# Kernel optimization log

Hardware: AMD Instinct MI355X
Metric: run time of the kernel (lower is better)

## Reference

```python
import jax, jax.numpy as jnp
import numpy as np

# Config (matches init_kwargs)
B, C, H, W = 32, 128, 12, 1200   # z: (B, in_dim, H, W)
DIN = C * H                       # 1536
FIX = 768                         # get_multiple(DIN // 2, 6)
OV = 4                            # overlap
G = 6                             # num_vqs
D = OV * FIX // G                 # 512 per-group embedding size (all equal)
K = 1024                          # codebook_size
COMMIT = 0.25


def setup_inputs() -> dict:
    key = jax.random.key(0)
    k1, k2, k3, k4 = jax.random.split(key, 4)
    z = jax.random.normal(k1, (B, C, H, W), dtype=jnp.float32)
    w_down = jax.random.normal(k2, (FIX, DIN), dtype=jnp.float32) * 0.02
    w_up = jax.random.normal(k3, (DIN, FIX), dtype=jnp.float32) * 0.02
    embedding = jax.random.normal(k4, (G, D, K), dtype=jnp.float32)  # per-group (embedding_size, num_embedding)
    return {"z": z, "w_down": w_down, "w_up": w_up, "embedding": embedding}


def _quantize_group(zg, emb):
    # zg: (B, T, D), emb: (D, K)
    zf = zg.reshape(-1, D)
    # squared euclidean distance: |z|^2 - 2 z@E + |E|^2 -> (N, K)
    dist = (zf * zf).sum(1, keepdims=True) - 2.0 * (zf @ emb) + (emb * emb).sum(0, keepdims=True)
    idx = jnp.argmin(dist, axis=1)            # (N,)
    q = jnp.take(emb.T, idx, axis=0).reshape(zg.shape)
    # straight-through estimator (training mode)
    zq = zg + jax.lax.stop_gradient(q - zg)
    loss = COMMIT * jnp.mean((jax.lax.stop_gradient(zq) - zg) ** 2)
    return zq, loss


def reference(z, w_down, w_up, embedding):
    # pre_process: (B,C,H,W) -> permute(0,2,3,1) -> permute(0,2,3,1) -> (B, W, C*H)
    x = jnp.transpose(z, (0, 3, 1, 2)).reshape(B, W, DIN)  # (B, W, C, H) flattened
    x = x @ w_down.T                                       # proj_down -> (B, W, FIX)
    T = W // OV
    x = x.reshape(B, T, OV * FIX)                          # (B, T, 3072)
    # split into G contiguous groups of size D along last axis -> (G, B, T, D)
    xg = jnp.transpose(x.reshape(B, T, G, D), (2, 0, 1, 3))
    zq_g, losses = jax.vmap(_quantize_group)(xg, embedding)
    vq_loss = losses.sum() / G
    # concat groups back -> (B, T, G*D)
    zq = jnp.transpose(zq_g, (1, 2, 0, 3)).reshape(B, T, G * D)
    # post_process: un-overlap, proj_up, back to (B, C, H, W)
    zq = zq.reshape(B, W, FIX)
    zq = zq @ w_up.T                                       # (B, W, DIN)
    zq = zq.reshape(B, W, C, H)
    zq = jnp.transpose(zq, (0, 3, 1, 2))                   # (B, H, W, C)
    zq = jnp.transpose(zq, (0, 3, 1, 2))                   # dim==4 -> (B, C, H, W)
    return zq, vq_loss
```

## Files before the change

kernel.cpp:

```cpp
#include <hip/hip_runtime.h>

#define BB 32
#define CC 128
#define HH 12
#define WW 1200
#define DIN 1536
#define FIXD 768
#define OVL 4
#define GG 6
#define DD 512
#define KK 1024
#define TT 300
#define NV 9600
#define MROWS 38400

#define Y_OFF     0
#define ET_OFF    29491200
#define NORM_OFF  32636928
#define BEST_OFF  32643072
#define LOSS_OFF  32758272
#define ZN_OFF    32758336
#define UMIN_OFF  32815936
#define CNT_OFF   32873536
#define MAXN_OFF  32931136
#define LIST_OFF  32931200
#define YBF_OFF   36617600
#define EBF_OFF   51363200

#define BSWZ(c) ((c) + 4 * ((c) >> 5))

typedef __attribute__((ext_vector_type(8))) short bf16x8;
typedef __attribute__((ext_vector_type(4))) float f32x4;

static __device__ inline unsigned short f2bf(float x) {
    unsigned u = __float_as_uint(x);
    unsigned r = (u + 0x7fffu + ((u >> 16) & 1u)) >> 16;
    return (unsigned short)r;
}
static __device__ inline unsigned enc32(float s) {
    unsigned u = __float_as_uint(s);
    return (u & 0x80000000u) ? ~u : (u | 0x80000000u);
}

__global__ __launch_bounds__(256) void k_gemm_down(const float* __restrict__ z,
                                                   const float* __restrict__ w_down,
                                                   float* __restrict__ Y) {
    __shared__ float As[16][132];
    __shared__ float Bs[16][140];
    const int n0 = blockIdx.y * 128, f0 = blockIdx.x * 128;
    const int tid = threadIdx.x;
    const int arow = tid & 127;
    const int ak0 = tid >> 7;
    const int nA = n0 + arow;
    const int bA = nA / WW, wA = nA - bA * WW;
    const size_t zbase = (size_t)bA * (CC * HH * WW) + wA;
    const int bcol = tid >> 1, bq = tid & 1;
    const int bsc = BSWZ(bcol);
    const int trow = tid >> 4, tcol = tid & 15;
    const int bread = tcol * 8 + 4 * (tcol >> 2);
    float acc[8][8] = {};
    for (int kt = 0; kt < DIN; kt += 16) {
        #pragma unroll
        for (int i = 0; i < 8; i++) {
            const int kk = ak0 + i * 2;
            As[kk][arow] = z[zbase + (size_t)(kt + kk) * WW];
        }
        #pragma unroll
        for (int i = 0; i < 2; i++) {
            const int q = bq + i * 2;
            const float4 v = *(const float4*)&w_down[(size_t)(f0 + bcol) * DIN + kt + q * 4];
            Bs[q * 4 + 0][bsc] = v.x;
            Bs[q * 4 + 1][bsc] = v.y;
            Bs[q * 4 + 2][bsc] = v.z;
            Bs[q * 4 + 3][bsc] = v.w;
        }
        __syncthreads();
        #pragma unroll
        for (int k = 0; k < 16; k++) {
            float av[8], bv[8];
            *(float4*)&av[0] = *(const float4*)&As[k][trow * 8];
            *(float4*)&av[4] = *(const float4*)&As[k][trow * 8 + 4];
            *(float4*)&bv[0] = *(const float4*)&Bs[k][bread];
            *(float4*)&bv[4] = *(const float4*)&Bs[k][bread + 4];
            #pragma unroll
            for (int i = 0; i < 8; i++)
                #pragma unroll
                for (int j = 0; j < 8; j++)
                    acc[i][j] = fmaf(av[i], bv[j], acc[i][j]);
        }
        __syncthreads();
    }
    #pragma unroll
    for (int i = 0; i < 8; i++) {
        float4 o0, o1;
        o0.x = acc[i][0]; o0.y = acc[i][1]; o0.z = acc[i][2]; o0.w = acc[i][3];
        o1.x = acc[i][4]; o1.y = acc[i][5]; o1.z = acc[i][6]; o1.w = acc[i][7];
        float* yr = &Y[(size_t)(n0 + trow * 8 + i) * FIXD + f0 + tcol * 8];
        *(float4*)yr = o0;
        *(float4*)(yr + 4) = o1;
    }
}

__global__ __launch_bounds__(256) void k_transpose(const float* __restrict__ emb,
                                                   float* __restrict__ ET) {
    int i = blockIdx.x * 256 + threadIdx.x;
    if (i >= GG * KK * DD) return;
    int d = i & 511;
    int rem = i >> 9;
    int k = rem & 1023;
    int g = rem >> 10;
    ET[i] = emb[((g * DD + d) << 10) + k];
}

__global__ __launch_bounds__(64) void k_norms(const float* __restrict__ ET,
                                              float* __restrict__ norms,
                                              unsigned* __restrict__ maxnU) {
    const int code = blockIdx.x;
    const int lane = threadIdx.x;
    const float* row = ET + code * DD;
    double s = 0.0;
    #pragma unroll
    for (int r = 0; r < 8; r++) {
        float v = row[lane + r * 64];
        s += (double)v * (double)v;
    }
    #pragma unroll
    for (int off = 32; off; off >>= 1) s += __shfl_down(s, off);
    if (lane == 0) {
        const float nf = (float)s;
        norms[code] = nf;
        atomicMax(&maxnU[code >> 10], __float_as_uint(nf));
    }
}

__global__ __launch_bounds__(256) void k_ysplit(const float* __restrict__ Y,
                                                unsigned short* __restrict__ Ybf,
                                                float* __restrict__ znorm) {
    const int gv = blockIdx.x * 4 + (threadIdx.x >> 6);
    const int lane = threadIdx.x & 63;
    const int g = gv / NV, r = gv - g * NV;
    const int b = r / TT, t = r - b * TT;
    const int d0 = lane * 8;
    const int p = g * DD + d0;
    const int sg = p / FIXD, f = p - sg * FIXD;
    const float* yb = &Y[(size_t)((b * WW + t * OVL + sg) * FIXD + f)];
    const float4 y0 = *(const float4*)yb;
    const float4 y1 = *(const float4*)(yb + 4);
    unsigned short h[8];
    h[0] = f2bf(y0.x); h[1] = f2bf(y0.y); h[2] = f2bf(y0.z); h[3] = f2bf(y0.w);
    h[4] = f2bf(y1.x); h[5] = f2bf(y1.y); h[6] = f2bf(y1.z); h[7] = f2bf(y1.w);
    *(uint4*)&Ybf[(size_t)gv * DD + d0] = *(uint4*)&h[0];
    float s = 0.f;
    s = fmaf(y0.x, y0.x, s); s = fmaf(y0.y, y0.y, s);
    s = fmaf(y0.z, y0.z, s); s = fmaf(y0.w, y0.w, s);
    s = fmaf(y1.x, y1.x, s); s = fmaf(y1.y, y1.y, s);
    s = fmaf(y1.z, y1.z, s); s = fmaf(y1.w, y1.w, s);
    #pragma unroll
    for (int off = 32; off; off >>= 1) s += __shfl_down(s, off);
    if (lane == 0) znorm[gv] = s;
}

__global__ __launch_bounds__(256) void k_esplit(const float* __restrict__ ET,
                                                unsigned short* __restrict__ Ebf) {
    const size_t i8 = ((size_t)blockIdx.x * 256 + threadIdx.x) * 8;
    const float4 a = *(const float4*)&ET[i8];
    const float4 b = *(const float4*)&ET[i8 + 4];
    unsigned short h[8];
    h[0] = f2bf(a.x); h[1] = f2bf(a.y); h[2] = f2bf(a.z); h[3] = f2bf(a.w);
    h[4] = f2bf(b.x); h[5] = f2bf(b.y); h[6] = f2bf(b.z); h[7] = f2bf(b.w);
    *(uint4*)&Ebf[i8] = *(uint4*)&h[0];
}

template<int PHASE>
__global__ __launch_bounds__(256) void k_dist3(const unsigned short* __restrict__ Ybf,
                                               const unsigned short* __restrict__ Ebf,
                                               const float* __restrict__ norms,
                                               const float* __restrict__ znorm,
                                               const unsigned* __restrict__ maxnU,
                                               unsigned* __restrict__ umin,
                                               unsigned* __restrict__ cnt,
                                               unsigned* __restrict__ list_) {
    __shared__ unsigned short Ah[128][40], Bh[128][40];
    __shared__ float a1s[128], margs[128];
    const int ct = blockIdx.x;
    const int vt = blockIdx.y;
    const int g  = blockIdx.z;
    const int v0 = vt * 128, c0 = ct * 128;
    const int tid = threadIdx.x;
    const size_t ybase = ((size_t)g * NV + v0) * DD;
    const size_t ebase = ((size_t)g * KK + c0) * DD;
    const int srow = tid >> 1, sseg = (tid & 1) * 16;
    const int wv = tid >> 6, lane = tid & 63;
    const int wr = wv >> 1, wc = wv & 1;
    const int m0 = wr * 64, n0 = wc * 64;
    const int lr = lane & 15, lq = lane >> 4;

    if (PHASE == 2 && tid < 128) {
        const int gv = g * NV + v0 + tid;
        const unsigned u = umin[gv];
        const unsigned x = (u & 0x80000000u) ? (u & 0x7fffffffu) : ~u;
        a1s[tid] = __uint_as_float(x);
        margs[tid] = 0.032f * sqrtf(znorm[gv] * __uint_as_float(maxnU[g]));
    }

    f32x4 acc[4][4];
    #pragma unroll
    for (int i = 0; i < 4; i++)
        #pragma unroll
        for (int j = 0; j < 4; j++) acc[i][j] = (f32x4){0.f, 0.f, 0.f, 0.f};

    for (int kt = 0; kt < DD; kt += 32) {
        {
            const uint4 a0 = *(const uint4*)&Ybf[ybase + (size_t)srow * DD + kt + sseg];
            const uint4 a1 = *(const uint4*)&Ybf[ybase + (size_t)srow * DD + kt + sseg + 8];
            const uint4 b0 = *(const uint4*)&Ebf[ebase + (size_t)srow * DD + kt + sseg];
            const uint4 b1 = *(const uint4*)&Ebf[ebase + (size_t)srow * DD + kt + sseg + 8];
            *(uint4*)&Ah[srow][sseg]     = a0;
            *(uint4*)&Ah[srow][sseg + 8] = a1;
            *(uint4*)&Bh[srow][sseg]     = b0;
            *(uint4*)&Bh[srow][sseg + 8] = b1;
        }
        __syncthreads();
        bf16x8 ah[4], bh[4];
        #pragma unroll
        for (int i = 0; i < 4; i++) {
            ah[i] = *(bf16x8*)&Ah[m0 + i * 16 + lr][lq * 8];
            bh[i] = *(bf16x8*)&Bh[n0 + i * 16 + lr][lq * 8];
        }
        #pragma unroll
        for (int i = 0; i < 4; i++)
            #pragma unroll
            for (int j = 0; j < 4; j++)
                acc[i][j] = __builtin_amdgcn_mfma_f32_16x16x32_bf16(ah[i], bh[j], acc[i][j], 0, 0, 0);
        __syncthreads();
    }

    float nrmj[4];
    #pragma unroll
    for (int j = 0; j < 4; j++) nrmj[j] = norms[(g << 10) + c0 + n0 + j * 16 + lr];

    #pragma unroll
    for (int i = 0; i < 4; i++) {
        #pragma unroll
        for (int rr = 0; rr < 4; rr++) {
            const int row = m0 + i * 16 + lq * 4 + rr;
            if (PHASE == 1) {
                unsigned kb = 0xFFFFFFFFu;
                #pragma unroll
                for (int j = 0; j < 4; j++) {
                    const unsigned u = enc32(nrmj[j] - 2.0f * acc[i][j][rr]);
                    kb = (u < kb) ? u : kb;
                }
                #pragma unroll
                for (int off = 1; off < 16; off <<= 1) {
                    const unsigned o = __shfl_xor(kb, off);
                    kb = (o < kb) ? o : kb;
                }
                if (lr == 0) atomicMin(&umin[g * NV + v0 + row], kb);
            } else {
                const float thr = a1s[row] + margs[row];
                #pragma unroll
                for (int j = 0; j < 4; j++) {
                    const float sc = nrmj[j] - 2.0f * acc[i][j][rr];
                    if (sc <= thr) {
                        const int gv = g * NV + v0 + row;
                        const unsigned idx = atomicAdd(&cnt[gv], 1u);
                        if (idx < 64u)
                            list_[(size_t)gv * 64 + idx] = (unsigned)(c0 + n0 + j * 16 + lr);
                    }
                }
            }
        }
    }
}

__global__ __launch_bounds__(64) void k_rescore(const float* __restrict__ Y,
                                                const float* __restrict__ ET,
                                                const float* __restrict__ norms,
                                                const unsigned* __restrict__ cnt,
                                                const unsigned* __restrict__ list_,
                                                unsigned long long* __restrict__ best) {
    const int gv = blockIdx.x;
    const unsigned n = cnt[gv];
    if (n == 0u || n > 64u) return;
    const int lane = threadIdx.x;
    const int g = gv / NV, r = gv - g * NV;
    const int b = r / TT, t = r - b * TT;
    unsigned long long key = ~0ull;
    if (lane < (int)n) {
        const unsigned c = list_[(size_t)gv * 64 + lane];
        const float* erow = &ET[((size_t)((g << 10) + c)) * DD];
        float s = 0.f;
        for (int d4 = 0; d4 < 128; ++d4) {
            const int p = g * DD + d4 * 4;
            const int sg = p / FIXD, f = p - sg * FIXD;
            const float4 yv = *(const float4*)&Y[(size_t)((b * WW + t * OVL + sg) * FIXD + f)];
            const float4 ev = *(const float4*)&erow[d4 * 4];
            s = fmaf(yv.x, ev.x, s); s = fmaf(yv.y, ev.y, s);
            s = fmaf(yv.z, ev.z, s); s = fmaf(yv.w, ev.w, s);
        }
        const float sc = norms[(g << 10) + c] - 2.0f * s;
        key = ((unsigned long long)enc32(sc) << 32) | c;
    }
    #pragma unroll
    for (int off = 32; off; off >>= 1) {
        const unsigned long long o = __shfl_down(key, off);
        if (o < key) key = o;
    }
    if (lane == 0) best[gv] = key;
}

__global__ __launch_bounds__(256) void k_fallback(const float* __restrict__ Y,
                                                  const float* __restrict__ ET,
                                                  const float* __restrict__ norms,
                                                  const unsigned* __restrict__ cnt,
                                                  unsigned long long* __restrict__ best) {
    const int gv = blockIdx.x;
    if (cnt[gv] <= 64u) return;
    __shared__ float Yv[512];
    __shared__ unsigned long long red[256];
    const int tid = threadIdx.x;
    const int g = gv / NV, r = gv - g * NV;
    const int b = r / TT, t = r - b * TT;
    if (tid < 128) {
        const int p = g * DD + tid * 4;
        const int sg = p / FIXD, f = p - sg * FIXD;
        *(float4*)&Yv[tid * 4] = *(const float4*)&Y[(size_t)((b * WW + t * OVL + sg) * FIXD + f)];
    }
    __syncthreads();
    unsigned long long kb = ~0ull;
    for (int cc = 0; cc < 4; ++cc) {
        const int c = tid + cc * 256;
        const float* erow = &ET[((size_t)((g << 10) + c)) * DD];
        float s = 0.f;
        for (int d = 0; d < 512; ++d) s = fmaf(Yv[d], erow[d], s);
        const float sc = norms[(g << 10) + c] - 2.0f * s;
        const unsigned long long key = ((unsigned long long)enc32(sc) << 32) | (unsigned)c;
        if (key < kb) kb = key;
    }
    red[tid] = kb;
    __syncthreads();
    for (int off = 128; off; off >>= 1) {
        if (tid < off) { if (red[tid + off] < red[tid]) red[tid] = red[tid + off]; }
        __syncthreads();
    }
    if (tid == 0) best[gv] = red[0];
}

__global__ __launch_bounds__(256) void k_sumloss(const unsigned long long* __restrict__ best,
                                                 const float* __restrict__ znorm,
                                                 float* __restrict__ lossAcc) {
    const int v = blockIdx.x * 256 + threadIdx.x;
    const unsigned long long key = best[v];
    const unsigned u = (unsigned)(key >> 32);
    const unsigned x = (u & 0x80000000u) ? (u & 0x7fffffffu) : ~u;
    float s = __uint_as_float(x) + znorm[v];
    __shared__ float red[256];
    red[threadIdx.x] = s;
    __syncthreads();
    for (int off = 128; off; off >>= 1) {
        if (threadIdx.x < off) red[threadIdx.x] += red[threadIdx.x + off];
        __syncthreads();
    }
    if (threadIdx.x == 0) atomicAdd(lossAcc, red[0]);
}

__constant__ int SEG_G[8]  = {0, 1, 1, 2, 3, 4, 4, 5};
__constant__ int SEG_D0[8] = {0, 0, 256, 0, 0, 0, 256, 0};
__constant__ int SEG_L[8]  = {512, 256, 256, 512, 512, 256, 256, 512};
__constant__ int SEG_F0[8] = {0, 512, 0, 256, 0, 512, 0, 256};

__global__ __launch_bounds__(256) void k_table(const float* __restrict__ ET,
                                               const float* __restrict__ w_up,
                                               float* __restrict__ Tab) {
    __shared__ float As[16][68];
    __shared__ float Bs[16][140];
    const int bm = blockIdx.x;
    const int bn = blockIdx.y;
    const int seg = blockIdx.z;
    const int g = SEG_G[seg], d0 = SEG_D0[seg], len = SEG_L[seg], fb = SEG_F0[seg];
    const int tid = threadIdx.x;
    const int k0 = bm * 64, dout0 = bn * 128;
    const int arow = tid >> 2, aq = tid & 3;
    const int rbase = (tid >> 4) << 2;
    const int cgrp = tid & 15;
    const int bread = cgrp * 8 + 4 * (cgrp >> 2);
    const float* ETg = ET + (size_t)(g << 10) * DD;
    float acc[4][8] = {};
    for (int kt = 0; kt < len; kt += 16) {
        {
            const float4 v = *(const float4*)&ETg[(size_t)(k0 + arow) * DD + d0 + kt + aq * 4];
            As[aq * 4 + 0][arow] = v.x;
            As[aq * 4 + 1][arow] = v.y;
            As[aq * 4 + 2][arow] = v.z;
            As[aq * 4 + 3][arow] = v.w;
        }
        #pragma unroll
        for (int i = 0; i < 2; i++) {
            int fl = tid + i * 256;
            int col = fl >> 2, q = fl & 3;
            const int sc = BSWZ(col);
            const float4 v = *(const float4*)&w_up[(size_t)(dout0 + col) * FIXD + fb + kt + q * 4];
            Bs[q * 4 + 0][sc] = v.x;
            Bs[q * 4 + 1][sc] = v.y;
            Bs[q * 4 + 2][sc] = v.z;
            Bs[q * 4 + 3][sc] = v.w;
        }
        __syncthreads();
        #pragma unroll
        for (int k = 0; k < 16; k++) {
            const float4 a  = *(const float4*)&As[k][rbase];
            const float4 ba = *(const float4*)&Bs[k][bread];
            const float4 bb = *(const float4*)&Bs[k][bread + 4];
            const float av[4] = {a.x, a.y, a.z, a.w};
            const float bv[8] = {ba.x, ba.y, ba.z, ba.w, bb.x, bb.y, bb.z, bb.w};
            #pragma unroll
            for (int i = 0; i < 4; i++)
                #pragma unroll
                for (int j = 0; j < 8; j++)
                    acc[i][j] = fmaf(av[i], bv[j], acc[i][j]);
        }
        __syncthreads();
    }
    #pragma unroll
    for (int i = 0; i < 4; i++) {
        float4 o0, o1;
        o0.x = acc[i][0]; o0.y = acc[i][1]; o0.z = acc[i][2]; o0.w = acc[i][3];
        o1.x = acc[i][4]; o1.y = acc[i][5]; o1.z = acc[i][6]; o1.w = acc[i][7];
        float* tr = &Tab[(size_t)((seg << 10) + k0 + rbase + i) * DIN + dout0 + cgrp * 8];
        *(float4*)tr = o0;
        *(float4*)(tr + 4) = o1;
    }
}

__global__ __launch_bounds__(256) void k_scatter(const float* __restrict__ Tab,
                                                 const unsigned long long* __restrict__ best,
                                                 float* __restrict__ out) {
    __shared__ float Ls[64][65];
    const int dt = blockIdx.x;
    const int wt = blockIdx.y;
    const int b  = blockIdx.z;
    const int dout0 = dt * 64, w0 = wt * 64;
    const int wlim = (WW - w0 < 64) ? (WW - w0) : 64;
    const int tid = threadIdx.x;
    const int wi = tid >> 2, q = tid & 3;

    if (wi < wlim) {
        const int w = w0 + wi;
        const int s = w & 3;
        const int t = w >> 2;
        const int gEt[4] = {0, 1, 3, 4};
        const int gOt[4] = {1, 2, 4, 5};
        int ce = (int)(unsigned)best[gEt[s] * NV + b * TT + t];
        int co = (int)(unsigned)best[gOt[s] * NV + b * TT + t];
        size_t rowE = (size_t)(((2 * s) << 10) + ce) * DIN;
        size_t rowO = (size_t)(((2 * s + 1) << 10) + co) * DIN;
        #pragma unroll
        for (int rep = 0; rep < 4; rep++) {
            const int doff = rep * 16 + q * 4;
            const float4 a = *(const float4*)&Tab[rowE + dout0 + doff];
            const float4 c = *(const float4*)&Tab[rowO + dout0 + doff];
            Ls[wi][doff + 0] = a.x + c.x;
            Ls[wi][doff + 1] = a.y + c.y;
            Ls[wi][doff + 2] = a.z + c.z;
            Ls[wi][doff + 3] = a.w + c.w;
        }
    }
    __syncthreads();
    const size_t obase = (size_t)b * (CC * HH * WW) + (size_t)dout0 * WW + w0;
    #pragma unroll
    for (int i = 0; i < 16; i++) {
        int flat = tid + i * 256;
        int dr = flat >> 6, wj = flat & 63;
        if (wj < wlim) out[obase + (size_t)dr * WW + wj] = Ls[wj][dr];
    }
}

__global__ void k_finish(const float* __restrict__ lossAcc, float* __restrict__ out) {
    if (threadIdx.x == 0)
        out[58982400] = lossAcc[0] * (0.25f / 29491200.0f);
}

extern "C" void kernel_launch(void* const* d_in, const int* in_sizes, int n_in,
                              void* d_out, int out_size, void* d_ws, size_t ws_size,
                              hipStream_t stream) {
    const float* z      = (const float*)d_in[0];
    const float* w_down = (const float*)d_in[1];
    const float* w_up   = (const float*)d_in[2];
    const float* emb    = (const float*)d_in[3];
    float* out = (float*)d_out;

    float* ws    = (float*)d_ws;
    float* Y     = ws + Y_OFF;
    float* Tab   = ws + Y_OFF;
    float* ET    = ws + ET_OFF;
    float* norms = ws + NORM_OFF;
    unsigned long long* best = (unsigned long long*)(ws + BEST_OFF);
    float* lossA = ws + LOSS_OFF;
    float* znorm = ws + ZN_OFF;
    unsigned* umin  = (unsigned*)(ws + UMIN_OFF);
    unsigned* cnt   = (unsigned*)(ws + CNT_OFF);
    unsigned* maxnU = (unsigned*)(ws + MAXN_OFF);
    unsigned* list_ = (unsigned*)(ws + LIST_OFF);
    unsigned short* Ybf = (unsigned short*)(ws + YBF_OFF);
    unsigned short* Ebf = (unsigned short*)(ws + EBF_OFF);

    hipMemsetAsync(best, 0xFF, (size_t)GG * NV * sizeof(unsigned long long), stream);
    hipMemsetAsync(umin, 0xFF, (size_t)GG * NV * sizeof(unsigned), stream);
    hipMemsetAsync(cnt, 0, (size_t)GG * NV * sizeof(unsigned), stream);
    hipMemsetAsync(maxnU, 0, 64, stream);
    hipMemsetAsync(lossA, 0, sizeof(float), stream);

    dim3 gdown(6, 300);
    k_gemm_down<<<gdown, 256, 0, stream>>>(z, w_down, Y);

    k_transpose<<<(GG * KK * DD + 255) / 256, 256, 0, stream>>>(emb, ET);
    k_norms<<<GG * KK, 64, 0, stream>>>(ET, norms, maxnU);

    k_ysplit<<<GG * NV / 4, 256, 0, stream>>>(Y, Ybf, znorm);
    k_esplit<<<GG * KK * DD / (256 * 8), 256, 0, stream>>>(ET, Ebf);

    dim3 gdist(8, 75, GG);
    k_dist3<1><<<gdist, 256, 0, stream>>>(Ybf, Ebf, norms, znorm, maxnU, umin, cnt, list_);
    k_dist3<2><<<gdist, 256, 0, stream>>>(Ybf, Ebf, norms, znorm, maxnU, umin, cnt, list_);

    k_rescore<<<GG * NV, 64, 0, stream>>>(Y, ET, norms, cnt, list_, best);
    k_fallback<<<GG * NV, 256, 0, stream>>>(Y, ET, norms, cnt, best);

    k_sumloss<<<225, 256, 0, stream>>>(best, znorm, lossA);

    dim3 gtab(16, 12, 8);
    k_table<<<gtab, 256, 0, stream>>>(ET, w_up, Tab);

    dim3 gsc(24, 19, 32);
    k_scatter<<<gsc, 256, 0, stream>>>(Tab, best, out);

    k_finish<<<1, 64, 0, stream>>>(lossA, out);
}
```

Before: 2.000 ms.

## Fuse two-pass distance search into one pass with per-tile local minimum thresholds

The two bf16 distance GEMM passes become one. The old first pass found a global per-row minimum via atomicMin, and a second pass recomputed the scores to collect candidates. Now each block reduces a row minimum over its own 128 codebook columns in shared memory and uses that as the filter threshold. This removes one full GEMM, the umin buffer and two memsets. The cost is that every column tile now contributes candidates, so each row gets at least eight. That means more rescore work and a higher chance of overflowing the 64-entry list into the slow fallback.

```diff
diff --git a/kernel.cpp b/kernel.cpp
--- a/kernel.cpp
+++ b/kernel.cpp
@@ -20,7 +20,6 @@
 #define BEST_OFF  32643072
 #define LOSS_OFF  32758272
 #define ZN_OFF    32758336
-#define UMIN_OFF  32815936
 #define CNT_OFF   32873536
 #define MAXN_OFF  32931136
 #define LIST_OFF  32931200
@@ -171,17 +170,17 @@
     *(uint4*)&Ebf[i8] = *(uint4*)&h[0];
 }
 
-template<int PHASE>
-__global__ __launch_bounds__(256) void k_dist3(const unsigned short* __restrict__ Ybf,
+__global__ __launch_bounds__(256) void k_dist4(const unsigned short* __restrict__ Ybf,
                                                const unsigned short* __restrict__ Ebf,
                                                const float* __restrict__ norms,
                                                const float* __restrict__ znorm,
                                                const unsigned* __restrict__ maxnU,
-                                               unsigned* __restrict__ umin,
                                                unsigned* __restrict__ cnt,
                                                unsigned* __restrict__ list_) {
     __shared__ unsigned short Ah[128][40], Bh[128][40];
-    __shared__ float a1s[128], margs[128];
+    __shared__ float margs[128];
+    __shared__ unsigned redmin[128][2];
+    __shared__ float thrs[128];
     const int ct = blockIdx.x;
     const int vt = blockIdx.y;
     const int g  = blockIdx.z;
@@ -195,11 +194,8 @@
     const int m0 = wr * 64, n0 = wc * 64;
     const int lr = lane & 15, lq = lane >> 4;
 
-    if (PHASE == 2 && tid < 128) {
+    if (tid < 128) {
         const int gv = g * NV + v0 + tid;
-        const unsigned u = umin[gv];
-        const unsigned x = (u & 0x80000000u) ? (u & 0x7fffffffu) : ~u;
-        a1s[tid] = __uint_as_float(x);
         margs[tid] = 0.032f * sqrtf(znorm[gv] * __uint_as_float(maxnU[g]));
     }
 
@@ -243,31 +239,43 @@
     for (int i = 0; i < 4; i++) {
         #pragma unroll
         for (int rr = 0; rr < 4; rr++) {
+            unsigned kb = 0xFFFFFFFFu;
+            #pragma unroll
+            for (int j = 0; j < 4; j++) {
+                const unsigned u = enc32(nrmj[j] - 2.0f * acc[i][j][rr]);
+                kb = (u < kb) ? u : kb;
+            }
+            #pragma unroll
+            for (int off = 1; off < 16; off <<= 1) {
+                const unsigned o = __shfl_xor(kb, off);
+                kb = (o < kb) ? o : kb;
+            }
+            if (lr == 0) redmin[m0 + i * 16 + lq * 4 + rr][wc] = kb;
+        }
+    }
+    __syncthreads();
+    if (tid < 128) {
+        const unsigned a = redmin[tid][0], b = redmin[tid][1];
+        const unsigned u = (a < b) ? a : b;
+        const unsigned x = (u & 0x80000000u) ? (u & 0x7fffffffu) : ~u;
+        thrs[tid] = __uint_as_float(x) + margs[tid];
+    }
+    __syncthreads();
+
+    #pragma unroll
+    for (int i = 0; i < 4; i++) {
+        #pragma unroll
+        for (int rr = 0; rr < 4; rr++) {
             const int row = m0 + i * 16 + lq * 4 + rr;
-            if (PHASE == 1) {
-                unsigned kb = 0xFFFFFFFFu;
-                #pragma unroll
-                for (int j = 0; j < 4; j++) {
-                    const unsigned u = enc32(nrmj[j] - 2.0f * acc[i][j][rr]);
-                    kb = (u < kb) ? u : kb;
-                }
-                #pragma unroll
-                for (int off = 1; off < 16; off <<= 1) {
-                    const unsigned o = __shfl_xor(kb, off);
-                    kb = (o < kb) ? o : kb;
-                }
-                if (lr == 0) atomicMin(&umin[g * NV + v0 + row], kb);
-            } else {
-                const float thr = a1s[row] + margs[row];
-                #pragma unroll
-                for (int j = 0; j < 4; j++) {
-                    const float sc = nrmj[j] - 2.0f * acc[i][j][rr];
-                    if (sc <= thr) {
-                        const int gv = g * NV + v0 + row;
-                        const unsigned idx = atomicAdd(&cnt[gv], 1u);
-                        if (idx < 64u)
-                            list_[(size_t)gv * 64 + idx] = (unsigned)(c0 + n0 + j * 16 + lr);
-                    }
+            const float thr = thrs[row];
+            #pragma unroll
+            for (int j = 0; j < 4; j++) {
+                const float sc = nrmj[j] - 2.0f * acc[i][j][rr];
+                if (sc <= thr) {
+                    const int gv = g * NV + v0 + row;
+                    const unsigned idx = atomicAdd(&cnt[gv], 1u);
+                    if (idx < 64u)
+                        list_[(size_t)gv * 64 + idx] = (unsigned)(c0 + n0 + j * 16 + lr);
                 }
             }
         }
@@ -282,7 +290,7 @@
                                                 unsigned long long* __restrict__ best) {
     const int gv = blockIdx.x;
     const unsigned n = cnt[gv];
-    if (n == 0u || n > 64u) return;
+    if (n > 64u) return;
     const int lane = threadIdx.x;
     const int g = gv / NV, r = gv - g * NV;
     const int b = r / TT, t = r - b * TT;
@@ -498,15 +506,12 @@
     unsigned long long* best = (unsigned long long*)(ws + BEST_OFF);
     float* lossA = ws + LOSS_OFF;
     float* znorm = ws + ZN_OFF;
-    unsigned* umin  = (unsigned*)(ws + UMIN_OFF);
     unsigned* cnt   = (unsigned*)(ws + CNT_OFF);
     unsigned* maxnU = (unsigned*)(ws + MAXN_OFF);
     unsigned* list_ = (unsigned*)(ws + LIST_OFF);
     unsigned short* Ybf = (unsigned short*)(ws + YBF_OFF);
     unsigned short* Ebf = (unsigned short*)(ws + EBF_OFF);
 
-    hipMemsetAsync(best, 0xFF, (size_t)GG * NV * sizeof(unsigned long long), stream);
-    hipMemsetAsync(umin, 0xFF, (size_t)GG * NV * sizeof(unsigned), stream);
     hipMemsetAsync(cnt, 0, (size_t)GG * NV * sizeof(unsigned), stream);
     hipMemsetAsync(maxnU, 0, 64, stream);
     hipMemsetAsync(lossA, 0, sizeof(float), stream);
@@ -521,8 +526,7 @@
     k_esplit<<<GG * KK * DD / (256 * 8), 256, 0, stream>>>(ET, Ebf);
 
     dim3 gdist(8, 75, GG);
-    k_dist3<1><<<gdist, 256, 0, stream>>>(Ybf, Ebf, norms, znorm, maxnU, umin, cnt, list_);
-    k_dist3<2><<<gdist, 256, 0, stream>>>(Ybf, Ebf, norms, znorm, maxnU, umin, cnt, list_);
+    k_dist4<<<gdist, 256, 0, stream>>>(Ybf, Ebf, norms, znorm, maxnU, cnt, list_);
 
     k_rescore<<<GG * NV, 64, 0, stream>>>(Y, ET, norms, cnt, list_, best);
     k_fallback<<<GG * NV, 256, 0, stream>>>(Y, ET, norms, cnt, best);
```

Result: no change. 2.010 ms, median of 2 (+0.5%).
